# Kernel tuning notes

Hardware: AMD Instinct MI355X
Metric: run time of the kernel (lower is better)

## Reference

```python
import jax, jax.numpy as jnp
import numpy as np

N, F, UNITS = 8192, 512, 128
EDGE_PROB = 0.004  # ~32 neighbors per node
NEG_INF = -1e10


def setup_inputs() -> dict:
    key = jax.random.key(0)
    ks = jax.random.split(key, 7)
    features = jax.random.normal(ks[0], (N, F), dtype=jnp.float32)
    A = (jax.random.uniform(ks[1], (N, N)) < EDGE_PROB).astype(jnp.float32)
    kernel = jax.random.normal(ks[2], (UNITS, F), dtype=jnp.float32) * (1.0 / np.sqrt(F))
    a_self = jax.random.normal(ks[3], (UNITS, 1), dtype=jnp.float32) * (1.0 / np.sqrt(UNITS))
    a_cross = jax.random.normal(ks[4], (UNITS, 1), dtype=jnp.float32) * (1.0 / np.sqrt(UNITS))
    dense_w = jax.random.normal(ks[5], (UNITS, UNITS), dtype=jnp.float32) * (1.0 / np.sqrt(UNITS))
    dense_b = jnp.zeros((UNITS,), dtype=jnp.float32)
    return {"features": features, "A": A, "kernel": kernel, "a_self": a_self,
            "a_cross": a_cross, "dense_w": dense_w, "dense_b": dense_b}


def reference(features, A, kernel, a_self, a_cross, dense_w, dense_b):
    # feature transform: [N, F] @ [F, units] -> [N, units]
    ft = features @ kernel.T
    s = ft @ a_self    # [N, 1]
    c = ft @ a_cross   # [N, 1]
    att = s + c.T      # [N, N] pairwise scores
    scores = jax.nn.leaky_relu(att, negative_slope=0.2)
    masked = scores + NEG_INF * (1.0 - A)
    sm = jax.nn.softmax(masked, axis=0)  # column-wise softmax (axis=0, as in TF code)
    out = sm @ ft                        # [N, units]
    # Flatten on [N, units] is identity; final Dense(units)
    return out @ dense_w + dense_b
```

## Files before the change

### kernel.cpp

```cpp
#include <hip/hip_runtime.h>
#include <math.h>


#define NND 8192
#define FFD 512
#define UUD 128
#define CAP 128

typedef float f32x4 __attribute__((ext_vector_type(4)));

__global__ __launch_bounds__(256) void k_ft(const float* __restrict__ feat,
                                            const float* __restrict__ ker,
                                            const float* __restrict__ a_self,
                                            const float* __restrict__ a_cross,
                                            float* __restrict__ ft,
                                            float* __restrict__ s,
                                            float* __restrict__ c) {
    __shared__ float As[32][20];
    __shared__ float Bs[32][132];
    const int tid = threadIdx.x;
    const int r0 = blockIdx.x * 16;
    const int tc = tid & 31;
    const int tr = tid >> 5;
    float acc[2][4];
#pragma unroll
    for (int x = 0; x < 2; x++)
#pragma unroll
        for (int y = 0; y < 4; y++) acc[x][y] = 0.f;

    for (int k0 = 0; k0 < FFD; k0 += 32) {
        __syncthreads();
        if (tid < 128) {
            int r = tid >> 3;
            int k4 = (tid & 7) << 2;
            f32x4 v = *(const f32x4*)&feat[(size_t)(r0 + r) * FFD + k0 + k4];
            As[k4 + 0][r] = v[0]; As[k4 + 1][r] = v[1];
            As[k4 + 2][r] = v[2]; As[k4 + 3][r] = v[3];
        }
#pragma unroll
        for (int it = 0; it < 4; it++) {
            int u = it * 32 + (tid >> 3);
            int k4 = (tid & 7) << 2;
            f32x4 v = *(const f32x4*)&ker[(size_t)u * FFD + k0 + k4];
            Bs[k4 + 0][u] = v[0]; Bs[k4 + 1][u] = v[1];
            Bs[k4 + 2][u] = v[2]; Bs[k4 + 3][u] = v[3];
        }
        __syncthreads();
#pragma unroll
        for (int kk = 0; kk < 32; kk++) {
            float a0 = As[kk][(tr << 1) + 0];
            float a1 = As[kk][(tr << 1) + 1];
            f32x4 b = *(const f32x4*)&Bs[kk][tc << 2];
#pragma unroll
            for (int y = 0; y < 4; y++) {
                acc[0][y] += a0 * b[y];
                acc[1][y] += a1 * b[y];
            }
        }
    }
#pragma unroll
    for (int x = 0; x < 2; x++) {
        int i = r0 + (tr << 1) + x;
        f32x4 v; v[0] = acc[x][0]; v[1] = acc[x][1]; v[2] = acc[x][2]; v[3] = acc[x][3];
        *(f32x4*)&ft[(size_t)i * UUD + (tc << 2)] = v;
    }

    f32x4 asv = *(const f32x4*)&a_self[tc << 2];
    f32x4 acv = *(const f32x4*)&a_cross[tc << 2];
#pragma unroll
    for (int x = 0; x < 2; x++) {
        float sv = acc[x][0] * asv[0] + acc[x][1] * asv[1] + acc[x][2] * asv[2] + acc[x][3] * asv[3];
        float cv = acc[x][0] * acv[0] + acc[x][1] * acv[1] + acc[x][2] * acv[2] + acc[x][3] * acv[3];
#pragma unroll
        for (int off = 16; off; off >>= 1) {
            sv += __shfl_xor(sv, off);
            cv += __shfl_xor(cv, off);
        }
        if (tc == 0) {
            int i = r0 + (tr << 1) + x;
            s[i] = sv; c[i] = cv;
        }
    }
}

__global__ __launch_bounds__(256) void k_scan(const float* __restrict__ A,
                                              const float* __restrict__ s,
                                              const float* __restrict__ c,
                                              int* __restrict__ row_cnt,
                                              int* __restrict__ edge_j,
                                              float* __restrict__ edge_w,
                                              float* __restrict__ denom) {
    __shared__ int cnt;
    const int i = blockIdx.x;
    const int tid = threadIdx.x;
    if (tid == 0) cnt = 0;
    __syncthreads();
    const float si = s[i];
    const f32x4* A4 = (const f32x4*)&A[(size_t)i * NND];
    f32x4 vv[8];
#pragma unroll
    for (int it = 0; it < 8; it++)
        vv[it] = __builtin_nontemporal_load(&A4[it * 256 + tid]);
#pragma unroll
    for (int it = 0; it < 8; it++) {
#pragma unroll
        for (int m = 0; m < 4; m++) {
            if (vv[it][m] != 0.f) {
                int j = ((it * 256 + tid) << 2) + m;
                float sc = si + c[j];
                sc = fmaxf(sc, 0.2f * sc);
                float w = expf(sc);
                int pos = atomicAdd(&cnt, 1);
                if (pos < CAP) {
                    edge_j[i * CAP + pos] = j;
                    edge_w[i * CAP + pos] = w;
                }
                atomicAdd(&denom[j], w);
            }
        }
    }
    __syncthreads();
    if (tid == 0) row_cnt[i] = (cnt < CAP) ? cnt : CAP;
}

__global__ __launch_bounds__(256) void k_z(const float* __restrict__ denom,
                                           const float* __restrict__ ft,
                                           float* __restrict__ zsum,
                                           int* __restrict__ zflag) {
    int j = blockIdx.x * 256 + threadIdx.x;
    if (denom[j] == 0.f) {
        atomicAdd(zflag, 1);
        for (int u = 0; u < UUD; u++) atomicAdd(&zsum[u], ft[(size_t)j * UUD + u]);
    }
}

__global__ __launch_bounds__(256) void k_agg_out(const int* __restrict__ row_cnt,
                                                 const int* __restrict__ edge_j,
                                                 const float* __restrict__ edge_w,
                                                 const float* __restrict__ denom,
                                                 const float* __restrict__ ft,
                                                 const float* __restrict__ zsum,
                                                 const int* __restrict__ zflag,
                                                 const float* __restrict__ W,
                                                 const float* __restrict__ bias,
                                                 float* __restrict__ out) {
    __shared__ int   jbuf[2][CAP];
    __shared__ float wbuf[2][CAP];
    __shared__ float rowpart[2][2][128];
    __shared__ float rowfull[2][128];
    const int tid = threadIdx.x;
    const int wv = tid >> 6;
    const int lane = tid & 63;
    const int r = wv >> 1;
    const int sub = wv & 1;
    const int i = blockIdx.x * 2 + r;
    const int cnt = row_cnt[i];

    {
        int e = sub * 64 + lane;
        if (e < cnt) {
            int j = edge_j[i * CAP + e];
            jbuf[r][e] = j;
            wbuf[r][e] = edge_w[i * CAP + e] / denom[j];
        }
    }
    __syncthreads();

    float acc0 = 0.f, acc1 = 0.f;
    for (int e = sub; e < cnt; e += 2) {
        int j = jbuf[r][e];
        float w = wbuf[r][e];
        acc0 += w * ft[(size_t)j * UUD + lane];
        acc1 += w * ft[(size_t)j * UUD + 64 + lane];
    }
    rowpart[r][sub][lane] = acc0;
    rowpart[r][sub][64 + lane] = acc1;
    __syncthreads();

    const int u = sub * 64 + lane;
    float agg = rowpart[r][0][u] + rowpart[r][1][u];
    if (*zflag) agg += (1.f / (float)NND) * zsum[u];
    rowfull[r][u] = agg;
    __syncthreads();

    float o = bias[u];
    for (int v = 0; v < UUD; v += 4) {
        f32x4 rv = *(const f32x4*)&rowfull[r][v];
#pragma unroll
        for (int mm = 0; mm < 4; mm++)
            o += rv[mm] * W[(size_t)(v + mm) * UUD + u];
    }
    out[(size_t)i * UUD + u] = o;
}

extern "C" void kernel_launch(void* const* d_in, const int* in_sizes, int n_in,
                              void* d_out, int out_size, void* d_ws, size_t ws_size,
                              hipStream_t stream) {
    const float* feat    = (const float*)d_in[0];
    const float* A       = (const float*)d_in[1];
    const float* ker     = (const float*)d_in[2];
    const float* a_self  = (const float*)d_in[3];
    const float* a_cross = (const float*)d_in[4];
    const float* W       = (const float*)d_in[5];
    const float* bias    = (const float*)d_in[6];
    float* out = (float*)d_out;

    char* p = (char*)d_ws;
    float* ft      = (float*)p;  p += (size_t)NND * UUD * 4;
    int*   edge_j  = (int*)p;    p += (size_t)NND * CAP * 4;
    float* edge_w  = (float*)p;  p += (size_t)NND * CAP * 4;
    float* s       = (float*)p;  p += NND * 4;
    float* c       = (float*)p;  p += NND * 4;
    int*   row_cnt = (int*)p;    p += NND * 4;
    float* denom   = (float*)p;  p += NND * 4;
    float* zsum    = (float*)p;  p += UUD * 4;
    int*   zflag   = (int*)p;    p += 4;

    hipMemsetAsync(denom, 0, (NND + UUD + 1) * 4, stream);

    k_ft<<<NND / 16, 256, 0, stream>>>(feat, ker, a_self, a_cross, ft, s, c);
    k_scan<<<NND, 256, 0, stream>>>(A, s, c, row_cnt, edge_j, edge_w, denom);
    k_z<<<NND / 256, 256, 0, stream>>>(denom, ft, zsum, zflag);
    k_agg_out<<<NND / 2, 256, 0, stream>>>(row_cnt, edge_j, edge_w, denom, ft,
                                           zsum, zflag, W, bias, out);
}
```

Before: 433.8 us.

## Compute attention scores via folded kernel vectors and overlap ft GEMM with adjacency scan

Folds a_self and a_cross into the projection weights (kernel^T·a), so s and c come straight from features in a small separate kernel. The ft GEMM and the adjacency scan then run in one launch as disjoint block ranges, letting the compute-bound GEMM overlap the bandwidth-bound scan of A. The memset is folded into the new kernel, which saves a launch. The cost is that every block of the small kernel recomputes the folded vectors and feat is read an extra time, and the change in summation order shifts the scores by rounding.

New measurement: 443.2 us. 1.02x slower.

```diff
diff --git a/kernel.cpp b/kernel.cpp
--- a/kernel.cpp
+++ b/kernel.cpp
@@ -6,121 +6,152 @@
 #define FFD 512
 #define UUD 128
 #define CAP 128
+#define FT_BLOCKS 512
 
 typedef float f32x4 __attribute__((ext_vector_type(4)));
 
-__global__ __launch_bounds__(256) void k_ft(const float* __restrict__ feat,
+__global__ __launch_bounds__(256) void k_sc(const float* __restrict__ feat,
                                             const float* __restrict__ ker,
                                             const float* __restrict__ a_self,
                                             const float* __restrict__ a_cross,
-                                            float* __restrict__ ft,
                                             float* __restrict__ s,
-                                            float* __restrict__ c) {
+                                            float* __restrict__ c,
+                                            float* __restrict__ zerobase) {
+    __shared__ float ks[FFD], kc[FFD];
+    const int tid = threadIdx.x;
+
+    {
+        int t = blockIdx.x * 256 + tid;
+        if (t < NND + UUD + 1) zerobase[t] = 0.f;
+    }
+
+    for (int f = tid; f < FFD; f += 256) {
+        float accs = 0.f, accc = 0.f;
+        for (int u = 0; u < UUD; u++) {
+            float kv = ker[(size_t)u * FFD + f];
+            accs += kv * a_self[u];
+            accc += kv * a_cross[u];
+        }
+        ks[f] = accs; kc[f] = accc;
+    }
+    __syncthreads();
+
+    const int wv = tid >> 6, lane = tid & 63;
+    const int i0 = blockIdx.x * 128 + wv * 32;
+    for (int rr = 0; rr < 32; rr++) {
+        int i = i0 + rr;
+        const f32x4* fr = (const f32x4*)&feat[(size_t)i * FFD];
+        f32x4 f0 = fr[lane * 2 + 0];
+        f32x4 f1 = fr[lane * 2 + 1];
+        f32x4 k0 = *(const f32x4*)&ks[lane * 8];
+        f32x4 k1 = *(const f32x4*)&ks[lane * 8 + 4];
+        f32x4 c0 = *(const f32x4*)&kc[lane * 8];
+        f32x4 c1 = *(const f32x4*)&kc[lane * 8 + 4];
+        float sv = f0[0]*k0[0] + f0[1]*k0[1] + f0[2]*k0[2] + f0[3]*k0[3]
+                 + f1[0]*k1[0] + f1[1]*k1[1] + f1[2]*k1[2] + f1[3]*k1[3];
+        float cv = f0[0]*c0[0] + f0[1]*c0[1] + f0[2]*c0[2] + f0[3]*c0[3]
+                 + f1[0]*c1[0] + f1[1]*c1[1] + f1[2]*c1[2] + f1[3]*c1[3];
+#pragma unroll
+        for (int off = 32; off; off >>= 1) {
+            sv += __shfl_xor(sv, off);
+            cv += __shfl_xor(cv, off);
+        }
+        if (lane == 0) { s[i] = sv; c[i] = cv; }
+    }
+}
+
+__global__ __launch_bounds__(256) void k_fused(const float* __restrict__ feat,
+                                               const float* __restrict__ ker,
+                                               const float* __restrict__ A,
+                                               const float* __restrict__ s,
+                                               const float* __restrict__ c,
+                                               float* __restrict__ ft,
+                                               int* __restrict__ row_cnt,
+                                               int* __restrict__ edge_j,
+                                               float* __restrict__ edge_w,
+                                               float* __restrict__ denom) {
     __shared__ float As[32][20];
     __shared__ float Bs[32][132];
+    __shared__ int cnt;
     const int tid = threadIdx.x;
-    const int r0 = blockIdx.x * 16;
-    const int tc = tid & 31;
-    const int tr = tid >> 5;
-    float acc[2][4];
-#pragma unroll
-    for (int x = 0; x < 2; x++)
-#pragma unroll
-        for (int y = 0; y < 4; y++) acc[x][y] = 0.f;
-
-    for (int k0 = 0; k0 < FFD; k0 += 32) {
+
+    if (blockIdx.x < FT_BLOCKS) {
+        const int r0 = blockIdx.x * 16;
+        const int tc = tid & 31;
+        const int tr = tid >> 5;
+        float acc[2][4];
+#pragma unroll
+        for (int x = 0; x < 2; x++)
+#pragma unroll
+            for (int y = 0; y < 4; y++) acc[x][y] = 0.f;
+
+        for (int k0 = 0; k0 < FFD; k0 += 32) {
+            __syncthreads();
+            if (tid < 128) {
+                int r = tid >> 3;
+                int k4 = (tid & 7) << 2;
+                f32x4 v = *(const f32x4*)&feat[(size_t)(r0 + r) * FFD + k0 + k4];
+                As[k4 + 0][r] = v[0]; As[k4 + 1][r] = v[1];
+                As[k4 + 2][r] = v[2]; As[k4 + 3][r] = v[3];
+            }
+#pragma unroll
+            for (int it = 0; it < 4; it++) {
+                int u = it * 32 + (tid >> 3);
+                int k4 = (tid & 7) << 2;
+                f32x4 v = *(const f32x4*)&ker[(size_t)u * FFD + k0 + k4];
+                Bs[k4 + 0][u] = v[0]; Bs[k4 + 1][u] = v[1];
+                Bs[k4 + 2][u] = v[2]; Bs[k4 + 3][u] = v[3];
+            }
+            __syncthreads();
+#pragma unroll
+            for (int kk = 0; kk < 32; kk++) {
+                float a0 = As[kk][(tr << 1) + 0];
+                float a1 = As[kk][(tr << 1) + 1];
+                f32x4 b = *(const f32x4*)&Bs[kk][tc << 2];
+#pragma unroll
+                for (int y = 0; y < 4; y++) {
+                    acc[0][y] += a0 * b[y];
+                    acc[1][y] += a1 * b[y];
+                }
+            }
+        }
+#pragma unroll
+        for (int x = 0; x < 2; x++) {
+            int i = r0 + (tr << 1) + x;
+            f32x4 v; v[0] = acc[x][0]; v[1] = acc[x][1]; v[2] = acc[x][2]; v[3] = acc[x][3];
+            *(f32x4*)&ft[(size_t)i * UUD + (tc << 2)] = v;
+        }
+    } else {
+        const int i = blockIdx.x - FT_BLOCKS;
+        if (tid == 0) cnt = 0;
         __syncthreads();
-        if (tid < 128) {
-            int r = tid >> 3;
-            int k4 = (tid & 7) << 2;
-            f32x4 v = *(const f32x4*)&feat[(size_t)(r0 + r) * FFD + k0 + k4];
-            As[k4 + 0][r] = v[0]; As[k4 + 1][r] = v[1];
-            As[k4 + 2][r] = v[2]; As[k4 + 3][r] = v[3];
-        }
-#pragma unroll
-        for (int it = 0; it < 4; it++) {
-            int u = it * 32 + (tid >> 3);
-            int k4 = (tid & 7) << 2;
-            f32x4 v = *(const f32x4*)&ker[(size_t)u * FFD + k0 + k4];
-            Bs[k4 + 0][u] = v[0]; Bs[k4 + 1][u] = v[1];
-            Bs[k4 + 2][u] = v[2]; Bs[k4 + 3][u] = v[3];
+        const float si = s[i];
+        const f32x4* A4 = (const f32x4*)&A[(size_t)i * NND];
+        f32x4 vv[8];
+#pragma unroll
+        for (int it = 0; it < 8; it++)
+            vv[it] = __builtin_nontemporal_load(&A4[it * 256 + tid]);
+#pragma unroll
+        for (int it = 0; it < 8; it++) {
+#pragma unroll
+            for (int m = 0; m < 4; m++) {
+                if (vv[it][m] != 0.f) {
+                    int j = ((it * 256 + tid) << 2) + m;
+                    float sc = si + c[j];
+                    sc = fmaxf(sc, 0.2f * sc);
+                    float w = expf(sc);
+                    int pos = atomicAdd(&cnt, 1);
+                    if (pos < CAP) {
+                        edge_j[i * CAP + pos] = j;
+                        edge_w[i * CAP + pos] = w;
+                    }
+                    atomicAdd(&denom[j], w);
+                }
+            }
         }
         __syncthreads();
-#pragma unroll
-        for (int kk = 0; kk < 32; kk++) {
-            float a0 = As[kk][(tr << 1) + 0];
-            float a1 = As[kk][(tr << 1) + 1];
-            f32x4 b = *(const f32x4*)&Bs[kk][tc << 2];
-#pragma unroll
-            for (int y = 0; y < 4; y++) {
-                acc[0][y] += a0 * b[y];
-                acc[1][y] += a1 * b[y];
-            }
-        }
-    }
-#pragma unroll
-    for (int x = 0; x < 2; x++) {
-        int i = r0 + (tr << 1) + x;
-        f32x4 v; v[0] = acc[x][0]; v[1] = acc[x][1]; v[2] = acc[x][2]; v[3] = acc[x][3];
-        *(f32x4*)&ft[(size_t)i * UUD + (tc << 2)] = v;
-    }
-
-    f32x4 asv = *(const f32x4*)&a_self[tc << 2];
-    f32x4 acv = *(const f32x4*)&a_cross[tc << 2];
-#pragma unroll
-    for (int x = 0; x < 2; x++) {
-        float sv = acc[x][0] * asv[0] + acc[x][1] * asv[1] + acc[x][2] * asv[2] + acc[x][3] * asv[3];
-        float cv = acc[x][0] * acv[0] + acc[x][1] * acv[1] + acc[x][2] * acv[2] + acc[x][3] * acv[3];
-#pragma unroll
-        for (int off = 16; off; off >>= 1) {
-            sv += __shfl_xor(sv, off);
-            cv += __shfl_xor(cv, off);
-        }
-        if (tc == 0) {
-            int i = r0 + (tr << 1) + x;
-            s[i] = sv; c[i] = cv;
-        }
-    }
-}
-
-__global__ __launch_bounds__(256) void k_scan(const float* __restrict__ A,
-                                              const float* __restrict__ s,
-                                              const float* __restrict__ c,
-                                              int* __restrict__ row_cnt,
-                                              int* __restrict__ edge_j,
-                                              float* __restrict__ edge_w,
-                                              float* __restrict__ denom) {
-    __shared__ int cnt;
-    const int i = blockIdx.x;
-    const int tid = threadIdx.x;
-    if (tid == 0) cnt = 0;
-    __syncthreads();
-    const float si = s[i];
-    const f32x4* A4 = (const f32x4*)&A[(size_t)i * NND];
-    f32x4 vv[8];
-#pragma unroll
-    for (int it = 0; it < 8; it++)
-        vv[it] = __builtin_nontemporal_load(&A4[it * 256 + tid]);
-#pragma unroll
-    for (int it = 0; it < 8; it++) {
-#pragma unroll
-        for (int m = 0; m < 4; m++) {
-            if (vv[it][m] != 0.f) {
-                int j = ((it * 256 + tid) << 2) + m;
-                float sc = si + c[j];
-                sc = fmaxf(sc, 0.2f * sc);
-                float w = expf(sc);
-                int pos = atomicAdd(&cnt, 1);
-                if (pos < CAP) {
-                    edge_j[i * CAP + pos] = j;
-                    edge_w[i * CAP + pos] = w;
-                }
-                atomicAdd(&denom[j], w);
-            }
-        }
-    }
-    __syncthreads();
-    if (tid == 0) row_cnt[i] = (cnt < CAP) ? cnt : CAP;
+        if (tid == 0) row_cnt[i] = (cnt < CAP) ? cnt : CAP;
+    }
 }
 
 __global__ __launch_bounds__(256) void k_z(const float* __restrict__ denom,
@@ -216,10 +247,9 @@
     float* zsum    = (float*)p;  p += UUD * 4;
     int*   zflag   = (int*)p;    p += 4;
 
-    hipMemsetAsync(denom, 0, (NND + UUD + 1) * 4, stream);
-
-    k_ft<<<NND / 16, 256, 0, stream>>>(feat, ker, a_self, a_cross, ft, s, c);
-    k_scan<<<NND, 256, 0, stream>>>(A, s, c, row_cnt, edge_j, edge_w, denom);
+    k_sc<<<64, 256, 0, stream>>>(feat, ker, a_self, a_cross, s, c, denom);
+    k_fused<<<FT_BLOCKS + NND, 256, 0, stream>>>(feat, ker, A, s, c, ft,
+                                                 row_cnt, edge_j, edge_w, denom);
     k_z<<<NND / 256, 256, 0, stream>>>(denom, ft, zsum, zflag);
     k_agg_out<<<NND / 2, 256, 0, stream>>>(row_cnt, edge_j, edge_w, denom, ft,
                                            zsum, zflag, W, bias, out);
```
